# Performance work log

Measured on AMD Instinct MI355X. Metric: run time of the kernel, lower is better.

## Reference

```python
import jax, jax.numpy as jnp
import numpy as np

HEADS = 4
DIM_HEAD = 32
SCALE = DIM_HEAD ** (-0.5)


def setup_inputs() -> dict:
    key = jax.random.key(0)
    k0, k1, k2 = jax.random.split(key, 3)
    B, C, H, W = 4, 256, 64, 64
    inner = HEADS * DIM_HEAD  # 128
    x = jax.random.normal(k0, (B, C, H, W), dtype=jnp.float32)
    # 1x1 conv weights reduce to matrices (out_ch, in_ch)
    w_qkv = jax.random.normal(k1, (3 * inner, C), dtype=jnp.float32) * 0.02
    w_out = jax.random.normal(k2, (C, inner), dtype=jnp.float32) * 0.02
    b_out = jnp.zeros((C,), dtype=jnp.float32)
    return {"x": x, "w_qkv": w_qkv, "w_out": w_out, "b_out": b_out}


def reference(x, w_qkv, w_out, b_out):
    b, c, h, w = x.shape
    n = h * w  # flattened spatial length
    inner = HEADS * DIM_HEAD
    # 1x1 conv == channel matmul: [b, 3*inner, h, w]
    qkv = jnp.einsum('oc,bchw->bohw', w_qkv, x)
    qkv = qkv.reshape(b, 3, HEADS, DIM_HEAD, n)  # split 3 * (heads dim_head)
    q, k, v = qkv[:, 0], qkv[:, 1], qkv[:, 2]    # each [b, heads, d, n]
    sim = jnp.einsum('bhdi,bhdj->bhij', q * SCALE, k)  # [b, h, n, n]
    attn = jax.nn.softmax(sim, axis=-1)  # stable (max-subtract) softmax
    out = jnp.einsum('bhij,bhdj->bhid', attn, v)       # [b, heads, n, d]
    # 'b h (x y) d -> b (h d) x y'
    out = out.transpose(0, 1, 3, 2).reshape(b, inner, h, w)
    y = jnp.einsum('oc,bchw->bohw', w_out, out) + b_out[None, :, None, None]
    return y
```

## Files before the change

kernel.cpp:

```cpp
#include <hip/hip_runtime.h>

#define N_TOK 4096
#define BATCH 4

typedef __attribute__((ext_vector_type(8))) short short8;
typedef __attribute__((ext_vector_type(4))) float floatx4;

__device__ __forceinline__ unsigned pack_rnd(float a, float b) {
    unsigned ra = __float_as_uint(a) + 0x8000u;
    unsigned rb = __float_as_uint(b) + 0x8000u;
    return __builtin_amdgcn_perm(rb, ra, 0x07060302u);
}

__device__ __forceinline__ void split_pack(float a, float b,
                                           unsigned &ph, unsigned &pl) {
    unsigned ra = __float_as_uint(a) + 0x8000u;
    unsigned rb = __float_as_uint(b) + 0x8000u;
    ph = __builtin_amdgcn_perm(rb, ra, 0x07060302u);
    float la = a - __uint_as_float(ra & 0xffff0000u);
    float lb = b - __uint_as_float(rb & 0xffff0000u);
    pl = __builtin_amdgcn_perm(__float_as_uint(lb) + 0x8000u,
                               __float_as_uint(la) + 0x8000u, 0x07060302u);
}

__device__ __forceinline__ short8 mk_short8(unsigned p0, unsigned p1,
                                            unsigned p2, unsigned p3) {
    union { unsigned u[4]; short8 s; } c;
    c.u[0] = p0; c.u[1] = p1; c.u[2] = p2; c.u[3] = p3;
    return c.s;
}

__device__ __forceinline__ void cvt_frag(const float* src,
                                         short8 &hi, short8 &lo) {
    float4 w0 = *(const float4*)src;
    float4 w1 = *(const float4*)(src + 4);
    unsigned ph[4], pl[4];
    split_pack(w0.x, w0.y, ph[0], pl[0]);
    split_pack(w0.z, w0.w, ph[1], pl[1]);
    split_pack(w1.x, w1.y, ph[2], pl[2]);
    split_pack(w1.z, w1.w, ph[3], pl[3]);
    hi = mk_short8(ph[0], ph[1], ph[2], ph[3]);
    lo = mk_short8(pl[0], pl[1], pl[2], pl[3]);
}

__device__ __forceinline__ float fast_exp2(float x) {
#if __has_builtin(__builtin_amdgcn_exp2f)
    return __builtin_amdgcn_exp2f(x);
#else
    return exp2f(x);
#endif
}

__global__ __launch_bounds__(256) void gemm1_fused(
    const float* __restrict__ wq, const float* __restrict__ x,
    unsigned short* __restrict__ Qp, unsigned short* __restrict__ Kp,
    unsigned short* __restrict__ Vp)
{
    const int N = N_TOK;
    const int b = blockIdx.z;
    const int row0 = blockIdx.y * 64;
    const int col0 = blockIdx.x * 64;
    const int t = threadIdx.x;
    const int wave = t >> 6, lane = t & 63;
    const int l16 = lane & 15, quad = lane >> 4;
    const int msub0 = (wave & 1) * 32, nsub0 = (wave >> 1) * 32;

    __shared__ __align__(16) char smem[20480];
    unsigned short* WsH = (unsigned short*)smem;
    unsigned short* WsL = (unsigned short*)(smem + 5120);
    unsigned short* XsH = (unsigned short*)(smem + 10240);
    unsigned short* XsL = (unsigned short*)(smem + 15360);

    floatx4 acc[2][2] = {};

    const int wm = t >> 2, wk = (t & 3) * 8;
    const int xn = t & 63, xc8 = (t >> 6) * 8;

    for (int kc = 0; kc < 8; ++kc) {
        __syncthreads();
        {
            const float* wsrc = wq + (size_t)(row0 + wm) * 256 + kc * 32 + wk;
            float4 w0 = *(const float4*)wsrc;
            float4 w1 = *(const float4*)(wsrc + 4);
            unsigned ph[4], pl[4];
            split_pack(w0.x, w0.y, ph[0], pl[0]);
            split_pack(w0.z, w0.w, ph[1], pl[1]);
            split_pack(w1.x, w1.y, ph[2], pl[2]);
            split_pack(w1.z, w1.w, ph[3], pl[3]);
            *(uint4*)(WsH + wm * 40 + wk) = *(uint4*)ph;
            *(uint4*)(WsL + wm * 40 + wk) = *(uint4*)pl;
        }
        {
            const float* xsrc = x + ((size_t)b * 256 + kc * 32 + xc8) * N
                                  + col0 + xn;
            float v[8];
#pragma unroll
            for (int i = 0; i < 8; ++i) v[i] = xsrc[(size_t)i * N];
            unsigned ph[4], pl[4];
            split_pack(v[0], v[1], ph[0], pl[0]);
            split_pack(v[2], v[3], ph[1], pl[1]);
            split_pack(v[4], v[5], ph[2], pl[2]);
            split_pack(v[6], v[7], ph[3], pl[3]);
            *(uint4*)(XsH + xn * 40 + xc8) = *(uint4*)ph;
            *(uint4*)(XsL + xn * 40 + xc8) = *(uint4*)pl;
        }
        __syncthreads();
        short8 ah0 = *(const short8*)(WsH + (msub0 + l16) * 40 + quad * 8);
        short8 ah1 = *(const short8*)(WsH + (msub0 + 16 + l16) * 40 + quad * 8);
        short8 al0 = *(const short8*)(WsL + (msub0 + l16) * 40 + quad * 8);
        short8 al1 = *(const short8*)(WsL + (msub0 + 16 + l16) * 40 + quad * 8);
        short8 bh0 = *(const short8*)(XsH + (nsub0 + l16) * 40 + quad * 8);
        short8 bh1 = *(const short8*)(XsH + (nsub0 + 16 + l16) * 40 + quad * 8);
        short8 bl0 = *(const short8*)(XsL + (nsub0 + l16) * 40 + quad * 8);
        short8 bl1 = *(const short8*)(XsL + (nsub0 + 16 + l16) * 40 + quad * 8);
        acc[0][0] = __builtin_amdgcn_mfma_f32_16x16x32_bf16(ah0, bh0, acc[0][0], 0, 0, 0);
        acc[0][1] = __builtin_amdgcn_mfma_f32_16x16x32_bf16(ah0, bh1, acc[0][1], 0, 0, 0);
        acc[1][0] = __builtin_amdgcn_mfma_f32_16x16x32_bf16(ah1, bh0, acc[1][0], 0, 0, 0);
        acc[1][1] = __builtin_amdgcn_mfma_f32_16x16x32_bf16(ah1, bh1, acc[1][1], 0, 0, 0);
        acc[0][0] = __builtin_amdgcn_mfma_f32_16x16x32_bf16(ah0, bl0, acc[0][0], 0, 0, 0);
        acc[0][1] = __builtin_amdgcn_mfma_f32_16x16x32_bf16(ah0, bl1, acc[0][1], 0, 0, 0);
        acc[1][0] = __builtin_amdgcn_mfma_f32_16x16x32_bf16(ah1, bl0, acc[1][0], 0, 0, 0);
        acc[1][1] = __builtin_amdgcn_mfma_f32_16x16x32_bf16(ah1, bl1, acc[1][1], 0, 0, 0);
        acc[0][0] = __builtin_amdgcn_mfma_f32_16x16x32_bf16(al0, bh0, acc[0][0], 0, 0, 0);
        acc[0][1] = __builtin_amdgcn_mfma_f32_16x16x32_bf16(al0, bh1, acc[0][1], 0, 0, 0);
        acc[1][0] = __builtin_amdgcn_mfma_f32_16x16x32_bf16(al1, bh0, acc[1][0], 0, 0, 0);
        acc[1][1] = __builtin_amdgcn_mfma_f32_16x16x32_bf16(al1, bh1, acc[1][1], 0, 0, 0);
    }

    __syncthreads();
    const int region = row0 >> 7;
    if (region == 2) {
        float (*LdsF)[68] = (float(*)[68])smem;
#pragma unroll
        for (int i = 0; i < 2; ++i)
#pragma unroll
            for (int j = 0; j < 2; ++j) {
                const int m = msub0 + i * 16 + quad * 4;
                const int n = nsub0 + j * 16 + l16;
#pragma unroll
                for (int r = 0; r < 4; ++r) LdsF[m + r][n] = acc[i][j][r];
            }
        __syncthreads();
        const int m = t >> 2, nb2 = (t & 3) * 16;
        const int vrow = b * 128 + (row0 - 256) + m;
        unsigned pk[8];
#pragma unroll
        for (int q = 0; q < 8; ++q)
            pk[q] = pack_rnd(LdsF[m][nb2 + 2 * q], LdsF[m][nb2 + 2 * q + 1]);
        unsigned short* dst = Vp + (size_t)vrow * N + col0 + nb2;
        *(uint4*)&dst[0] = *(uint4*)&pk[0];
        *(uint4*)&dst[8] = *(uint4*)&pk[4];
    } else {
        unsigned short (*LdsT)[68] = (unsigned short(*)[68])smem;
        const float sc = region ? 1.0f
                                : (0.17677669529663687f * 1.4426950408889634f);
#pragma unroll
        for (int i = 0; i < 2; ++i)
#pragma unroll
            for (int j = 0; j < 2; ++j) {
                const int m = msub0 + i * 16 + quad * 4;
                const int n = nsub0 + j * 16 + l16;
                uint2 pr;
                pr.x = pack_rnd(acc[i][j][0] * sc, acc[i][j][1] * sc);
                pr.y = pack_rnd(acc[i][j][2] * sc, acc[i][j][3] * sc);
                *(uint2*)&LdsT[n][m] = pr;
            }
        __syncthreads();
        const int n = t & 63, hb = (t >> 6) & 1, dh = t >> 7;
        const int h = ((row0 & 127) >> 5) + hb;
        const int m0 = hb * 32 + dh * 16;
        unsigned tmp[8];
        *(uint2*)&tmp[0] = *(const uint2*)&LdsT[n][m0];
        *(uint2*)&tmp[2] = *(const uint2*)&LdsT[n][m0 + 4];
        *(uint2*)&tmp[4] = *(const uint2*)&LdsT[n][m0 + 8];
        *(uint2*)&tmp[6] = *(const uint2*)&LdsT[n][m0 + 12];
        unsigned short* dst = (region ? Kp : Qp) +
            ((size_t)(b * 4 + h) * N + col0 + n) * 32 + dh * 16;
        *(uint4*)&dst[0] = *(uint4*)&tmp[0];
        *(uint4*)&dst[8] = *(uint4*)&tmp[4];
    }
}

__global__ __launch_bounds__(512) void attn_fused(
    const unsigned short* __restrict__ Qp,
    const unsigned short* __restrict__ Kp,
    const unsigned short* __restrict__ Vp,
    unsigned short* __restrict__ Oth, unsigned short* __restrict__ Otl)
{
    const int N = N_TOK;
    const int bh = blockIdx.y;
    const int b = bh >> 2, h = bh & 3;
    const int i0 = blockIdx.x * 128;
    const int t = threadIdx.x;
    const int wave = t >> 6, lane = t & 63;
    const int l16 = lane & 15, quad = lane >> 4;
    const int team = wave >> 2, w4 = wave & 3;

    __shared__ __align__(16) char smem[38912];
    unsigned short* S = (unsigned short*)smem;

    short8 ones;
#pragma unroll
    for (int e = 0; e < 8; ++e) ones[e] = (short)0x3F80;

    short8 qh[2];
#pragma unroll
    for (int g = 0; g < 2; ++g)
        qh[g] = *(const short8*)(Qp +
            ((size_t)bh * N + i0 + w4 * 32 + g * 16 + l16) * 32 + quad * 8);

    floatx4 o[2][2] = {};
    floatx4 lacc[2] = {};

    const int st_k = t & 255;
    const int skey = st_k >> 2, sdp = (st_k & 3) * 8;
    const int sslot = (skey & 32) | ((skey & 4) << 2) | ((skey & 24) >> 1)
                    | (skey & 3);
    const int svd = st_k >> 3, svp = (st_k & 7) * 8;
    const unsigned short* kp0 = Kp + ((size_t)bh * N + skey) * 32 + sdp;
    const unsigned short* kp1 = kp0 + (size_t)2048 * 32;
    const unsigned short* vp0 = Vp + ((size_t)bh * 32 + svd) * N + svp;
    const unsigned short* vp1 = vp0 + 2048;

    short8 r0, r1;
    if (t < 256) { r0 = *(const short8*)kp0; r1 = *(const short8*)kp1; }
    else         { r0 = *(const short8*)vp0; r1 = *(const short8*)vp1; }
    if (t < 256) {
        *(short8*)(S + sslot * 40 + sdp) = r0;
        *(short8*)(S + 2560 + sslot * 40 + sdp) = r1;
    } else {
        *(short8*)(S + 10240 + svd * 72 + svp) = r0;
        *(short8*)(S + 10240 + 2304 + svd * 72 + svp) = r1;
    }
    kp0 += 64 * 32; kp1 += 64 * 32; vp0 += 64; vp1 += 64;
    if (t < 256) { r0 = *(const short8*)kp0; r1 = *(const short8*)kp1; }
    else         { r0 = *(const short8*)vp0; r1 = *(const short8*)vp1; }
    __syncthreads();

    for (int it = 0; it < 32; ++it) {
        const int cur = it & 1;
        if (it + 1 < 32) {
            const int nb = 1 - cur;
            if (t < 256) {
                *(short8*)(S + nb * 5120 + sslot * 40 + sdp) = r0;
                *(short8*)(S + nb * 5120 + 2560 + sslot * 40 + sdp) = r1;
            } else {
                *(short8*)(S + 10240 + nb * 4608 + svd * 72 + svp) = r0;
                *(short8*)(S + 10240 + nb * 4608 + 2304 + svd * 72 + svp) = r1;
            }
        }
        if (it + 2 < 32) {
            kp0 += 64 * 32; kp1 += 64 * 32; vp0 += 64; vp1 += 64;
            if (t < 256) { r0 = *(const short8*)kp0; r1 = *(const short8*)kp1; }
            else         { r0 = *(const short8*)vp0; r1 = *(const short8*)vp1; }
        }

        const unsigned short* Ksr = S + cur * 5120 + team * 2560;
        const unsigned short* Vsr = S + 10240 + cur * 4608 + team * 2304;

        short8 kh0 = *(const short8*)(Ksr + ( 0 + l16) * 40 + quad * 8);
        short8 kh1 = *(const short8*)(Ksr + (16 + l16) * 40 + quad * 8);
        short8 kh2 = *(const short8*)(Ksr + (32 + l16) * 40 + quad * 8);
        short8 kh3 = *(const short8*)(Ksr + (48 + l16) * 40 + quad * 8);
        short8 vh00 = *(const short8*)(Vsr + ( 0 + l16) * 72 +  0 + quad * 8);
        short8 vh01 = *(const short8*)(Vsr + (16 + l16) * 72 +  0 + quad * 8);
        short8 vh10 = *(const short8*)(Vsr + ( 0 + l16) * 72 + 32 + quad * 8);
        short8 vh11 = *(const short8*)(Vsr + (16 + l16) * 72 + 32 + quad * 8);

#pragma unroll
        for (int g = 0; g < 2; ++g) {
            const floatx4 z = {0.0f, 0.0f, 0.0f, 0.0f};
            floatx4 s0 = __builtin_amdgcn_mfma_f32_16x16x32_bf16(kh0, qh[g], z, 0, 0, 0);
            floatx4 s1 = __builtin_amdgcn_mfma_f32_16x16x32_bf16(kh1, qh[g], z, 0, 0, 0);
            floatx4 s2 = __builtin_amdgcn_mfma_f32_16x16x32_bf16(kh2, qh[g], z, 0, 0, 0);
            floatx4 s3 = __builtin_amdgcn_mfma_f32_16x16x32_bf16(kh3, qh[g], z, 0, 0, 0);
            short8 pf0 = mk_short8(
                pack_rnd(fast_exp2(s0[0]), fast_exp2(s0[1])),
                pack_rnd(fast_exp2(s0[2]), fast_exp2(s0[3])),
                pack_rnd(fast_exp2(s1[0]), fast_exp2(s1[1])),
                pack_rnd(fast_exp2(s1[2]), fast_exp2(s1[3])));
            o[g][0] = __builtin_amdgcn_mfma_f32_16x16x32_bf16(vh00, pf0, o[g][0], 0, 0, 0);
            o[g][1] = __builtin_amdgcn_mfma_f32_16x16x32_bf16(vh01, pf0, o[g][1], 0, 0, 0);
            lacc[g] = __builtin_amdgcn_mfma_f32_16x16x32_bf16(ones, pf0, lacc[g], 0, 0, 0);
            short8 pf1 = mk_short8(
                pack_rnd(fast_exp2(s2[0]), fast_exp2(s2[1])),
                pack_rnd(fast_exp2(s2[2]), fast_exp2(s2[3])),
                pack_rnd(fast_exp2(s3[0]), fast_exp2(s3[1])),
                pack_rnd(fast_exp2(s3[2]), fast_exp2(s3[3])));
            o[g][0] = __builtin_amdgcn_mfma_f32_16x16x32_bf16(vh10, pf1, o[g][0], 0, 0, 0);
            o[g][1] = __builtin_amdgcn_mfma_f32_16x16x32_bf16(vh11, pf1, o[g][1], 0, 0, 0);
            lacc[g] = __builtin_amdgcn_mfma_f32_16x16x32_bf16(ones, pf1, lacc[g], 0, 0, 0);
        }
        __syncthreads();
    }

    float (*OfB)[132] = (float(*)[132])smem;
    float* Lb = (float*)(smem + 16896);
    float (*OfA)[132] = (float(*)[132])(smem + 17408);

    if (team == 1) {
#pragma unroll
        for (int g = 0; g < 2; ++g) {
            const int q = w4 * 32 + g * 16 + l16;
#pragma unroll
            for (int half = 0; half < 2; ++half)
#pragma unroll
                for (int r = 0; r < 4; ++r)
                    OfB[half * 16 + quad * 4 + r][q] = o[g][half][r];
            if (quad == 0) Lb[q] = lacc[g][0];
        }
    }
    __syncthreads();
    if (team == 0) {
#pragma unroll
        for (int g = 0; g < 2; ++g) {
            const int q = w4 * 32 + g * 16 + l16;
            const float inv = 1.0f / (lacc[g][0] + Lb[q]);
#pragma unroll
            for (int half = 0; half < 2; ++half)
#pragma unroll
                for (int r = 0; r < 4; ++r) {
                    const int d = half * 16 + quad * 4 + r;
                    OfA[d][q] = (o[g][half][r] + OfB[d][q]) * inv;
                }
        }
    }
    __syncthreads();
    {
        const int q = t >> 2, db = (t & 3) * 8;
        unsigned ph[4], pl[4];
#pragma unroll
        for (int i = 0; i < 4; ++i)
            split_pack(OfA[db + 2 * i][q], OfA[db + 2 * i + 1][q], ph[i], pl[i]);
        const size_t off = ((size_t)b * N + i0 + q) * 128 + h * 32 + db;
        *(uint4*)(Oth + off) = *(uint4*)ph;
        *(uint4*)(Otl + off) = *(uint4*)pl;
    }
}

__global__ __launch_bounds__(256) void gemm2_fused(
    const float* __restrict__ wo,
    const unsigned short* __restrict__ Oth, const unsigned short* __restrict__ Otl,
    const float* __restrict__ bias, float* __restrict__ y)
{
    const int N = N_TOK;
    const int b = blockIdx.z;
    const int row0 = blockIdx.y * 64;
    const int col0 = blockIdx.x * 64;
    const int t = threadIdx.x;
    const int wave = t >> 6, lane = t & 63;
    const int l16 = lane & 15, quad = lane >> 4;
    const int msub0 = (wave & 1) * 32, nsub0 = (wave >> 1) * 32;

    __shared__ __align__(16) char smem[17408];
    unsigned short* BsH = (unsigned short*)smem;
    unsigned short* BsL = (unsigned short*)(smem + 5120);
    float (*LdsF)[68] = (float(*)[68])smem;

    short8 ah[4][2], al[4][2];
#pragma unroll
    for (int kc = 0; kc < 4; ++kc)
#pragma unroll
        for (int r = 0; r < 2; ++r)
            cvt_frag(wo + (size_t)(row0 + msub0 + r * 16 + l16) * 128 +
                         kc * 32 + quad * 8,
                     ah[kc][r], al[kc][r]);

    const int srow = t >> 2, sk = (t & 3) * 8;
    const unsigned short* gH = Oth + ((size_t)b * N + col0 + srow) * 128 + sk;
    const unsigned short* gL = Otl + ((size_t)b * N + col0 + srow) * 128 + sk;

    floatx4 acc[2][2] = {};
#pragma unroll
    for (int kc = 0; kc < 4; ++kc) {
        short8 hreg = *(const short8*)(gH + kc * 32);
        short8 lreg = *(const short8*)(gL + kc * 32);
        __syncthreads();
        *(short8*)(BsH + srow * 40 + sk) = hreg;
        *(short8*)(BsL + srow * 40 + sk) = lreg;
        __syncthreads();
        short8 bh0 = *(const short8*)(BsH + (nsub0 + l16) * 40 + quad * 8);
        short8 bh1 = *(const short8*)(BsH + (nsub0 + 16 + l16) * 40 + quad * 8);
        short8 bl0 = *(const short8*)(BsL + (nsub0 + l16) * 40 + quad * 8);
        short8 bl1 = *(const short8*)(BsL + (nsub0 + 16 + l16) * 40 + quad * 8);
        acc[0][0] = __builtin_amdgcn_mfma_f32_16x16x32_bf16(ah[kc][0], bh0, acc[0][0], 0, 0, 0);
        acc[0][1] = __builtin_amdgcn_mfma_f32_16x16x32_bf16(ah[kc][0], bh1, acc[0][1], 0, 0, 0);
        acc[1][0] = __builtin_amdgcn_mfma_f32_16x16x32_bf16(ah[kc][1], bh0, acc[1][0], 0, 0, 0);
        acc[1][1] = __builtin_amdgcn_mfma_f32_16x16x32_bf16(ah[kc][1], bh1, acc[1][1], 0, 0, 0);
        acc[0][0] = __builtin_amdgcn_mfma_f32_16x16x32_bf16(ah[kc][0], bl0, acc[0][0], 0, 0, 0);
        acc[0][1] = __builtin_amdgcn_mfma_f32_16x16x32_bf16(ah[kc][0], bl1, acc[0][1], 0, 0, 0);
        acc[1][0] = __builtin_amdgcn_mfma_f32_16x16x32_bf16(ah[kc][1], bl0, acc[1][0], 0, 0, 0);
        acc[1][1] = __builtin_amdgcn_mfma_f32_16x16x32_bf16(ah[kc][1], bl1, acc[1][1], 0, 0, 0);
        acc[0][0] = __builtin_amdgcn_mfma_f32_16x16x32_bf16(al[kc][0], bh0, acc[0][0], 0, 0, 0);
        acc[0][1] = __builtin_amdgcn_mfma_f32_16x16x32_bf16(al[kc][0], bh1, acc[0][1], 0, 0, 0);
        acc[1][0] = __builtin_amdgcn_mfma_f32_16x16x32_bf16(al[kc][1], bh0, acc[1][0], 0, 0, 0);
        acc[1][1] = __builtin_amdgcn_mfma_f32_16x16x32_bf16(al[kc][1], bh1, acc[1][1], 0, 0, 0);
    }

    __syncthreads();
#pragma unroll
    for (int i = 0; i < 2; ++i)
#pragma unroll
        for (int j = 0; j < 2; ++j) {
            const int m = msub0 + i * 16 + quad * 4;
            const int n = nsub0 + j * 16 + l16;
#pragma unroll
            for (int r = 0; r < 4; ++r) LdsF[m + r][n] = acc[i][j][r];
        }
    __syncthreads();
    const int m = t >> 2, nb = (t & 3) * 16;
    const float bv = bias[row0 + m];
    float* dst = y + ((size_t)b * 256 + row0 + m) * N + col0 + nb;
#pragma unroll
    for (int g = 0; g < 4; ++g) {
        float4 o4;
        o4.x = LdsF[m][nb + g * 4 + 0] + bv;
        o4.y = LdsF[m][nb + g * 4 + 1] + bv;
        o4.z = LdsF[m][nb + g * 4 + 2] + bv;
        o4.w = LdsF[m][nb + g * 4 + 3] + bv;
        *(float4*)(dst + g * 4) = o4;
    }
}

extern "C" void kernel_launch(void* const* d_in, const int* in_sizes, int n_in,
                              void* d_out, int out_size, void* d_ws, size_t ws_size,
                              hipStream_t stream) {
    const float* x     = (const float*)d_in[0];
    const float* w_qkv = (const float*)d_in[1];
    const float* w_out = (const float*)d_in[2];
    const float* b_out = (const float*)d_in[3];
    float* y = (float*)d_out;

    char* base = (char*)d_ws;
    unsigned short* Qp  = (unsigned short*)base;
    unsigned short* Kp  = Qp + (size_t)16 * N_TOK * 32;
    unsigned short* Vp  = Kp + (size_t)16 * N_TOK * 32;
    unsigned short* Oth = Vp + (size_t)16 * N_TOK * 32;
    unsigned short* Otl = Oth + (size_t)BATCH * N_TOK * 128;

    gemm1_fused<<<dim3(64, 6, BATCH), dim3(256), 0, stream>>>(
        w_qkv, x, Qp, Kp, Vp);
    attn_fused<<<dim3(32, 16), dim3(512), 0, stream>>>(Qp, Kp, Vp, Oth, Otl);
    gemm2_fused<<<dim3(64, 4, BATCH), dim3(256), 0, stream>>>(
        w_out, Oth, Otl, b_out, y);
}
```

Measured before the change: 152.5 us.

## Double-buffer LDS tiles with register prefetch in both projection GEMMs

The QKV projection GEMM now double-buffers its LDS tiles. It prefetches the next K-chunk of weights and activations into registers while MFMAs run on the current buffer, which leaves one barrier per iteration instead of two. The output projection GEMM loads all four K-chunks of its bf16 operands into registers up front and ping-pongs them through two LDS buffers. This is meant to hide global load latency behind matrix math, at the cost of doubled LDS use and more registers, which may lower occupancy.

```diff
diff --git a/kernel.cpp b/kernel.cpp
--- a/kernel.cpp
+++ b/kernel.cpp
@@ -65,54 +65,58 @@
     const int l16 = lane & 15, quad = lane >> 4;
     const int msub0 = (wave & 1) * 32, nsub0 = (wave >> 1) * 32;
 
-    __shared__ __align__(16) char smem[20480];
-    unsigned short* WsH = (unsigned short*)smem;
-    unsigned short* WsL = (unsigned short*)(smem + 5120);
-    unsigned short* XsH = (unsigned short*)(smem + 10240);
-    unsigned short* XsL = (unsigned short*)(smem + 15360);
-
-    floatx4 acc[2][2] = {};
+    __shared__ __align__(16) char smem[40960];
+    unsigned short* S = (unsigned short*)smem;
 
     const int wm = t >> 2, wk = (t & 3) * 8;
     const int xn = t & 63, xc8 = (t >> 6) * 8;
 
+    const float* wbase = wq + (size_t)(row0 + wm) * 256 + wk;
+    const float* xbase = x + ((size_t)b * 256 + xc8) * N + col0 + xn;
+
+    floatx4 acc[2][2] = {};
+
+    float4 rw0 = *(const float4*)wbase;
+    float4 rw1 = *(const float4*)(wbase + 4);
+    float rx[8];
+#pragma unroll
+    for (int i = 0; i < 8; ++i) rx[i] = xbase[(size_t)i * N];
+    {
+        unsigned ph[4], pl[4];
+        split_pack(rw0.x, rw0.y, ph[0], pl[0]);
+        split_pack(rw0.z, rw0.w, ph[1], pl[1]);
+        split_pack(rw1.x, rw1.y, ph[2], pl[2]);
+        split_pack(rw1.z, rw1.w, ph[3], pl[3]);
+        *(uint4*)(S +        wm * 40 + wk) = *(uint4*)ph;
+        *(uint4*)(S + 2560 + wm * 40 + wk) = *(uint4*)pl;
+        split_pack(rx[0], rx[1], ph[0], pl[0]);
+        split_pack(rx[2], rx[3], ph[1], pl[1]);
+        split_pack(rx[4], rx[5], ph[2], pl[2]);
+        split_pack(rx[6], rx[7], ph[3], pl[3]);
+        *(uint4*)(S + 5120 + xn * 40 + xc8) = *(uint4*)ph;
+        *(uint4*)(S + 7680 + xn * 40 + xc8) = *(uint4*)pl;
+    }
+    __syncthreads();
+
     for (int kc = 0; kc < 8; ++kc) {
-        __syncthreads();
-        {
-            const float* wsrc = wq + (size_t)(row0 + wm) * 256 + kc * 32 + wk;
-            float4 w0 = *(const float4*)wsrc;
-            float4 w1 = *(const float4*)(wsrc + 4);
-            unsigned ph[4], pl[4];
-            split_pack(w0.x, w0.y, ph[0], pl[0]);
-            split_pack(w0.z, w0.w, ph[1], pl[1]);
-            split_pack(w1.x, w1.y, ph[2], pl[2]);
-            split_pack(w1.z, w1.w, ph[3], pl[3]);
-            *(uint4*)(WsH + wm * 40 + wk) = *(uint4*)ph;
-            *(uint4*)(WsL + wm * 40 + wk) = *(uint4*)pl;
-        }
-        {
-            const float* xsrc = x + ((size_t)b * 256 + kc * 32 + xc8) * N
-                                  + col0 + xn;
-            float v[8];
-#pragma unroll
-            for (int i = 0; i < 8; ++i) v[i] = xsrc[(size_t)i * N];
-            unsigned ph[4], pl[4];
-            split_pack(v[0], v[1], ph[0], pl[0]);
-            split_pack(v[2], v[3], ph[1], pl[1]);
-            split_pack(v[4], v[5], ph[2], pl[2]);
-            split_pack(v[6], v[7], ph[3], pl[3]);
-            *(uint4*)(XsH + xn * 40 + xc8) = *(uint4*)ph;
-            *(uint4*)(XsL + xn * 40 + xc8) = *(uint4*)pl;
-        }
-        __syncthreads();
-        short8 ah0 = *(const short8*)(WsH + (msub0 + l16) * 40 + quad * 8);
-        short8 ah1 = *(const short8*)(WsH + (msub0 + 16 + l16) * 40 + quad * 8);
-        short8 al0 = *(const short8*)(WsL + (msub0 + l16) * 40 + quad * 8);
-        short8 al1 = *(const short8*)(WsL + (msub0 + 16 + l16) * 40 + quad * 8);
-        short8 bh0 = *(const short8*)(XsH + (nsub0 + l16) * 40 + quad * 8);
-        short8 bh1 = *(const short8*)(XsH + (nsub0 + 16 + l16) * 40 + quad * 8);
-        short8 bl0 = *(const short8*)(XsL + (nsub0 + l16) * 40 + quad * 8);
-        short8 bl1 = *(const short8*)(XsL + (nsub0 + 16 + l16) * 40 + quad * 8);
+        const int cur = kc & 1;
+        if (kc + 1 < 8) {
+            const float* wsrc = wbase + (kc + 1) * 32;
+            rw0 = *(const float4*)wsrc;
+            rw1 = *(const float4*)(wsrc + 4);
+            const float* xsrc = xbase + (size_t)(kc + 1) * 32 * N;
+#pragma unroll
+            for (int i = 0; i < 8; ++i) rx[i] = xsrc[(size_t)i * N];
+        }
+        const unsigned short* B0 = S + cur * 10240;
+        short8 ah0 = *(const short8*)(B0 +        (msub0 +      l16) * 40 + quad * 8);
+        short8 ah1 = *(const short8*)(B0 +        (msub0 + 16 + l16) * 40 + quad * 8);
+        short8 al0 = *(const short8*)(B0 + 2560 + (msub0 +      l16) * 40 + quad * 8);
+        short8 al1 = *(const short8*)(B0 + 2560 + (msub0 + 16 + l16) * 40 + quad * 8);
+        short8 bh0 = *(const short8*)(B0 + 5120 + (nsub0 +      l16) * 40 + quad * 8);
+        short8 bh1 = *(const short8*)(B0 + 5120 + (nsub0 + 16 + l16) * 40 + quad * 8);
+        short8 bl0 = *(const short8*)(B0 + 7680 + (nsub0 +      l16) * 40 + quad * 8);
+        short8 bl1 = *(const short8*)(B0 + 7680 + (nsub0 + 16 + l16) * 40 + quad * 8);
         acc[0][0] = __builtin_amdgcn_mfma_f32_16x16x32_bf16(ah0, bh0, acc[0][0], 0, 0, 0);
         acc[0][1] = __builtin_amdgcn_mfma_f32_16x16x32_bf16(ah0, bh1, acc[0][1], 0, 0, 0);
         acc[1][0] = __builtin_amdgcn_mfma_f32_16x16x32_bf16(ah1, bh0, acc[1][0], 0, 0, 0);
@@ -125,9 +129,25 @@
         acc[0][1] = __builtin_amdgcn_mfma_f32_16x16x32_bf16(al0, bh1, acc[0][1], 0, 0, 0);
         acc[1][0] = __builtin_amdgcn_mfma_f32_16x16x32_bf16(al1, bh0, acc[1][0], 0, 0, 0);
         acc[1][1] = __builtin_amdgcn_mfma_f32_16x16x32_bf16(al1, bh1, acc[1][1], 0, 0, 0);
-    }
-
-    __syncthreads();
+        if (kc + 1 < 8) {
+            unsigned short* D = S + (1 - cur) * 10240;
+            unsigned ph[4], pl[4];
+            split_pack(rw0.x, rw0.y, ph[0], pl[0]);
+            split_pack(rw0.z, rw0.w, ph[1], pl[1]);
+            split_pack(rw1.x, rw1.y, ph[2], pl[2]);
+            split_pack(rw1.z, rw1.w, ph[3], pl[3]);
+            *(uint4*)(D +        wm * 40 + wk) = *(uint4*)ph;
+            *(uint4*)(D + 2560 + wm * 40 + wk) = *(uint4*)pl;
+            split_pack(rx[0], rx[1], ph[0], pl[0]);
+            split_pack(rx[2], rx[3], ph[1], pl[1]);
+            split_pack(rx[4], rx[5], ph[2], pl[2]);
+            split_pack(rx[6], rx[7], ph[3], pl[3]);
+            *(uint4*)(D + 5120 + xn * 40 + xc8) = *(uint4*)ph;
+            *(uint4*)(D + 7680 + xn * 40 + xc8) = *(uint4*)pl;
+        }
+        __syncthreads();
+    }
+
     const int region = row0 >> 7;
     if (region == 2) {
         float (*LdsF)[68] = (float(*)[68])smem;
@@ -352,10 +372,20 @@
     const int l16 = lane & 15, quad = lane >> 4;
     const int msub0 = (wave & 1) * 32, nsub0 = (wave >> 1) * 32;
 
-    __shared__ __align__(16) char smem[17408];
-    unsigned short* BsH = (unsigned short*)smem;
-    unsigned short* BsL = (unsigned short*)(smem + 5120);
+    __shared__ __align__(16) char smem[20480];
+    unsigned short* S = (unsigned short*)smem;
     float (*LdsF)[68] = (float(*)[68])smem;
+
+    const int srow = t >> 2, sk = (t & 3) * 8;
+    const unsigned short* gH = Oth + ((size_t)b * N + col0 + srow) * 128 + sk;
+    const unsigned short* gL = Otl + ((size_t)b * N + col0 + srow) * 128 + sk;
+
+    short8 hr[4], lr[4];
+#pragma unroll
+    for (int kc = 0; kc < 4; ++kc) {
+        hr[kc] = *(const short8*)(gH + kc * 32);
+        lr[kc] = *(const short8*)(gL + kc * 32);
+    }
 
     short8 ah[4][2], al[4][2];
 #pragma unroll
@@ -366,23 +396,19 @@
                          kc * 32 + quad * 8,
                      ah[kc][r], al[kc][r]);
 
-    const int srow = t >> 2, sk = (t & 3) * 8;
-    const unsigned short* gH = Oth + ((size_t)b * N + col0 + srow) * 128 + sk;
-    const unsigned short* gL = Otl + ((size_t)b * N + col0 + srow) * 128 + sk;
+    *(short8*)(S +        srow * 40 + sk) = hr[0];
+    *(short8*)(S + 2560 + srow * 40 + sk) = lr[0];
+    __syncthreads();
 
     floatx4 acc[2][2] = {};
 #pragma unroll
     for (int kc = 0; kc < 4; ++kc) {
-        short8 hreg = *(const short8*)(gH + kc * 32);
-        short8 lreg = *(const short8*)(gL + kc * 32);
-        __syncthreads();
-        *(short8*)(BsH + srow * 40 + sk) = hreg;
-        *(short8*)(BsL + srow * 40 + sk) = lreg;
-        __syncthreads();
-        short8 bh0 = *(const short8*)(BsH + (nsub0 + l16) * 40 + quad * 8);
-        short8 bh1 = *(const short8*)(BsH + (nsub0 + 16 + l16) * 40 + quad * 8);
-        short8 bl0 = *(const short8*)(BsL + (nsub0 + l16) * 40 + quad * 8);
-        short8 bl1 = *(const short8*)(BsL + (nsub0 + 16 + l16) * 40 + quad * 8);
+        const int cur = kc & 1;
+        const unsigned short* B0 = S + cur * 5120;
+        short8 bh0 = *(const short8*)(B0 +        (nsub0 +      l16) * 40 + quad * 8);
+        short8 bh1 = *(const short8*)(B0 +        (nsub0 + 16 + l16) * 40 + quad * 8);
+        short8 bl0 = *(const short8*)(B0 + 2560 + (nsub0 +      l16) * 40 + quad * 8);
+        short8 bl1 = *(const short8*)(B0 + 2560 + (nsub0 + 16 + l16) * 40 + quad * 8);
         acc[0][0] = __builtin_amdgcn_mfma_f32_16x16x32_bf16(ah[kc][0], bh0, acc[0][0], 0, 0, 0);
         acc[0][1] = __builtin_amdgcn_mfma_f32_16x16x32_bf16(ah[kc][0], bh1, acc[0][1], 0, 0, 0);
         acc[1][0] = __builtin_amdgcn_mfma_f32_16x16x32_bf16(ah[kc][1], bh0, acc[1][0], 0, 0, 0);
@@ -395,9 +421,14 @@
         acc[0][1] = __builtin_amdgcn_mfma_f32_16x16x32_bf16(al[kc][0], bh1, acc[0][1], 0, 0, 0);
         acc[1][0] = __builtin_amdgcn_mfma_f32_16x16x32_bf16(al[kc][1], bh0, acc[1][0], 0, 0, 0);
         acc[1][1] = __builtin_amdgcn_mfma_f32_16x16x32_bf16(al[kc][1], bh1, acc[1][1], 0, 0, 0);
-    }
-
-    __syncthreads();
+        if (kc + 1 < 4) {
+            unsigned short* D = S + (1 - cur) * 5120;
+            *(short8*)(D +        srow * 40 + sk) = hr[kc + 1];
+            *(short8*)(D + 2560 + srow * 40 + sk) = lr[kc + 1];
+        }
+        __syncthreads();
+    }
+
 #pragma unroll
     for (int i = 0; i < 2; ++i)
 #pragma unroll
```

Result: no change. 155.2 us (+1.7%).
